# Kernel tuning notes

Measured on AMD Instinct MI355X. Metric: run time of the kernel, lower is better.

## Reference

```python
import jax, jax.numpy as jnp
import numpy as np

T, D = 2048, 2048
N = 16
DN, DR, DV = 128, 64, 128   # qk_nope_head_dim, qk_rope_head_dim, v_head_dim
RQ, RKV = 1536, 512         # q_lora_rank, kv_lora_rank
EPS = 1e-6
THETA = 10000.0


def rmsnorm(x, scale, eps=EPS):
    var = jnp.mean(jnp.square(x), axis=-1, keepdims=True)
    return x * jax.lax.rsqrt(var + eps) * scale


def apply_rope(x, pos, theta=THETA):
    # x: [T, dr] or [T, N, dr]; rotate-half (NeoX) rotary embedding
    dr = x.shape[-1]
    half = dr // 2
    inv_freq = theta ** (-jnp.arange(half, dtype=jnp.float32) / half)
    freqs = pos.astype(jnp.float32)[:, None] * inv_freq  # [T, half]
    cos, sin = jnp.cos(freqs), jnp.sin(freqs)
    while cos.ndim < x.ndim:
        cos, sin = cos[:, None, :], sin[:, None, :]
    x1, x2 = jnp.split(x, 2, axis=-1)
    return jnp.concatenate([x1 * cos - x2 * sin, x2 * cos + x1 * sin], axis=-1).astype(x.dtype)


def setup_inputs() -> dict:
    key = jax.random.key(0)
    ks = jax.random.split(key, 6)
    s = 0.02
    return {
        'x': jax.random.normal(ks[0], (T, D), jnp.float32),
        'positions': jnp.arange(T, dtype=jnp.int32),
        'w_q_a': jax.random.normal(ks[1], (D, RQ), jnp.float32) * s,
        'q_a_norm': jnp.ones((RQ,), jnp.float32),
        'w_q_b': jax.random.normal(ks[2], (RQ, N * (DN + DR)), jnp.float32) * s,
        'w_kv_a': jax.random.normal(ks[3], (D, RKV + DR), jnp.float32) * s,
        'kv_a_norm': jnp.ones((RKV,), jnp.float32),
        'w_kv_b': jax.random.normal(ks[4], (RKV, N * (DN + DV)), jnp.float32) * s,
        'w_o': jax.random.normal(ks[5], (N * DV, D), jnp.float32) * s,
    }


def reference(x, positions, w_q_a, q_a_norm, w_q_b, w_kv_a, kv_a_norm, w_kv_b, w_o):
    t = x.shape[0]
    # --- low-rank Q projection ---
    q_c = rmsnorm(x @ w_q_a, q_a_norm)                      # [T, RQ]
    q = (q_c @ w_q_b).reshape(t, N, DN + DR)                # [T, N, DN+DR]
    q_nope, q_pe = q[..., :DN], q[..., DN:]
    q_pe = apply_rope(q_pe, positions)                      # [T, N, DR]
    # --- low-rank KV projection with shared rope key (MQA-style k_pe) ---
    kv = x @ w_kv_a                                          # [T, RKV+DR]
    kv_c, k_pe = kv[:, :RKV], kv[:, RKV:]
    kv_c = rmsnorm(kv_c, kv_a_norm)                          # [T, RKV]
    k_pe = apply_rope(k_pe, positions)                       # [T, DR]
    kvb = (kv_c @ w_kv_b).reshape(t, N, DN + DV)             # [T, N, DN+DV]
    k_nope, v = kvb[..., :DN], kvb[..., DN:]
    # --- causal attention, scale over full qk head dim ---
    scale = (DN + DR) ** -0.5
    scores = (jnp.einsum('tnh,snh->nts', q_nope, k_nope)
              + jnp.einsum('tnh,sh->nts', q_pe, k_pe)) * scale   # [N, T, T]
    causal = positions[:, None] >= positions[None, :]
    scores = jnp.where(causal[None, :, :], scores, jnp.finfo(scores.dtype).min)
    p = jax.nn.softmax(scores, axis=-1)
    out = jnp.einsum('nts,snv->tnv', p, v).reshape(t, N * DV)
    return out @ w_o                                          # [T, D]
```

## Files before the change

### kernel.cpp

```cpp
#include <hip/hip_runtime.h>
#include <hip/hip_bf16.h>
#include <math.h>

#define T_TOK   2048
#define NHEADS  16
#define EPS_    1e-6f
#define THETA_  10000.0f

typedef __attribute__((ext_vector_type(8))) short short8v;
typedef __attribute__((ext_vector_type(4))) float f32x4;

__device__ inline unsigned short f2bf(float f) {
    union { float f; unsigned u; } v; v.f = f;
    unsigned r = v.u + 0x7fffu + ((v.u >> 16) & 1u);
    return (unsigned short)(r >> 16);
}

__device__ __forceinline__ void gload16(const unsigned short* src, unsigned short* lds) {
    __builtin_amdgcn_global_load_lds(
        (const __attribute__((address_space(1))) unsigned int*)src,
        (__attribute__((address_space(3))) unsigned int*)lds, 16, 0, 0);
}

__device__ inline float block_reduce(float v, bool is_max, float* sred) {
    #pragma unroll
    for (int off = 32; off > 0; off >>= 1) {
        float o = __shfl_down(v, off, 64);
        v = is_max ? fmaxf(v, o) : (v + o);
    }
    int tid = threadIdx.x;
    __syncthreads();
    if ((tid & 63) == 0) sred[tid >> 6] = v;
    __syncthreads();
    float r = sred[0];
    #pragma unroll
    for (int w = 1; w < 4; ++w) r = is_max ? fmaxf(r, sred[w]) : (r + sred[w]);
    return r;
}

__global__ __launch_bounds__(256) void conv_bf16(const float* __restrict__ in,
    unsigned short* __restrict__ out, int n4)
{
    int i = blockIdx.x * 256 + threadIdx.x;
    if (i >= n4) return;
    float4 v = ((const float4*)in)[i];
    ushort4 o;
    o.x = f2bf(v.x); o.y = f2bf(v.y); o.z = f2bf(v.z); o.w = f2bf(v.w);
    ((ushort4*)out)[i] = o;
}

__global__ __launch_bounds__(256) void wt_bf16(const float* __restrict__ W,
    unsigned short* __restrict__ Wt, int R, int C)
{
    __shared__ float tile[32][33];
    int c0 = blockIdx.x * 32, r0 = blockIdx.y * 32;
    int tx = threadIdx.x & 31, ty = threadIdx.x >> 5;
    #pragma unroll
    for (int i = 0; i < 4; ++i)
        tile[ty + i * 8][tx] = W[(size_t)(r0 + ty + i * 8) * C + c0 + tx];
    __syncthreads();
    #pragma unroll
    for (int i = 0; i < 4; ++i)
        Wt[(size_t)(c0 + ty + i * 8) * R + r0 + tx] = f2bf(tile[tx][ty + i * 8]);
}

template<bool BF16OUT>
__global__ __launch_bounds__(256) void gemm_bf16(
    const unsigned short* __restrict__ A,
    const unsigned short* __restrict__ Bt,
    void* __restrict__ Cv, int N, int K, int ldc)
{
    __shared__ __align__(16) unsigned short As[2][128 * 64];
    __shared__ __align__(16) unsigned short Bs[2][128 * 64];
    const int tid = threadIdx.x;
    const int lane = tid & 63, wid = tid >> 6;
    const int wr = wid >> 1, wc = wid & 1;
    const int lrow = lane & 15, lkg = lane >> 4;
    const int r0 = blockIdx.y * 128, c0 = blockIdx.x * 128;

    f32x4 acc[4][4];
    #pragma unroll
    for (int m = 0; m < 4; ++m)
        #pragma unroll
        for (int n = 0; n < 4; ++n) acc[m][n] = (f32x4)0.f;

    #define STAGE_GEMM(buf, k0)                                                   \
        {   _Pragma("unroll")                                                     \
            for (int p = 0; p < 4; ++p) {                                         \
                int u = p * 256 + tid;                                            \
                int r = u >> 3, cu = u & 7;                                       \
                int dst = (p * 256 + wid * 64) * 8;                               \
                gload16(A  + (size_t)(r0 + r) * K + (k0) + ((cu ^ (r & 7)) << 3), \
                        As[buf] + dst);                                           \
                gload16(Bt + (size_t)(c0 + r) * K + (k0) + ((cu ^ (r & 7)) << 3), \
                        Bs[buf] + dst);                                           \
            }                                                                     \
        }

    STAGE_GEMM(0, 0)

    const int nkt = K >> 6;
    int buf = 0;
    for (int kt = 0; kt < nkt; ++kt) {
        if (kt + 1 < nkt) {
            STAGE_GEMM(buf ^ 1, (kt + 1) << 6)
            asm volatile("s_waitcnt vmcnt(8)" ::: "memory");
        } else {
            asm volatile("s_waitcnt vmcnt(0)" ::: "memory");
        }
        __builtin_amdgcn_s_barrier();
        #pragma unroll
        for (int ks = 0; ks < 2; ++ks) {
            short8v af[4], bf[4];
            #pragma unroll
            for (int m = 0; m < 4; ++m) {
                int row = wr * 64 + m * 16 + lrow;
                af[m] = *(const short8v*)((char*)As[buf] + row * 128 + (((ks * 4 + lkg) ^ (row & 7)) << 4));
            }
            #pragma unroll
            for (int n = 0; n < 4; ++n) {
                int row = wc * 64 + n * 16 + lrow;
                bf[n] = *(const short8v*)((char*)Bs[buf] + row * 128 + (((ks * 4 + lkg) ^ (row & 7)) << 4));
            }
            #pragma unroll
            for (int m = 0; m < 4; ++m)
                #pragma unroll
                for (int n = 0; n < 4; ++n)
                    acc[m][n] = __builtin_amdgcn_mfma_f32_16x16x32_bf16(af[m], bf[n], acc[m][n], 0, 0, 0);
        }
        __builtin_amdgcn_s_barrier();
        buf ^= 1;
    }
    #undef STAGE_GEMM

    #pragma unroll
    for (int m = 0; m < 4; ++m) {
        int grow = r0 + wr * 64 + m * 16 + lkg * 4;
        #pragma unroll
        for (int n = 0; n < 4; ++n) {
            int gcol = c0 + wc * 64 + n * 16 + lrow;
            if (gcol < N) {
                #pragma unroll
                for (int j = 0; j < 4; ++j) {
                    if (BF16OUT)
                        ((unsigned short*)Cv)[(size_t)(grow + j) * ldc + gcol] = f2bf(acc[m][n][j]);
                    else
                        ((float*)Cv)[(size_t)(grow + j) * ldc + gcol] = acc[m][n][j];
                }
            }
        }
    }
}

__global__ __launch_bounds__(256) void rms_kv(const float* __restrict__ qkv,
    const float* __restrict__ gq, const float* __restrict__ gkv,
    const int* __restrict__ positions, unsigned short* __restrict__ q_cb,
    unsigned short* __restrict__ kv_cb, float* __restrict__ kpe)
{
    __shared__ float sred[4];
    int row = blockIdx.x, tid = threadIdx.x;
    const float* p = qkv + (size_t)row * 2112;

    float ss = 0.f;
    for (int i = tid; i < 1536; i += 256) { float v = p[i]; ss += v * v; }
    ss = block_reduce(ss, false, sred);
    float sc = rsqrtf(ss / 1536.0f + EPS_);
    for (int i = tid; i < 1536; i += 256)
        q_cb[(size_t)row * 1536 + i] = f2bf(p[i] * sc * gq[i]);

    float s2 = 0.f;
    for (int i = tid; i < 512; i += 256) { float v = p[1536 + i]; s2 += v * v; }
    s2 = block_reduce(s2, false, sred);
    float sc2 = rsqrtf(s2 / 512.0f + EPS_);
    for (int i = tid; i < 512; i += 256)
        kv_cb[(size_t)row * 512 + i] = f2bf(p[1536 + i] * sc2 * gkv[i]);

    if (tid < 32) {
        int i = tid;
        float pos = (float)positions[row];
        float inv = powf(THETA_, -(float)i / 32.0f);
        float ang = pos * inv;
        float c = cosf(ang), s = sinf(ang);
        float x1 = p[2048 + i], x2 = p[2080 + i];
        kpe[(size_t)row * 64 + i]      = x1 * c - x2 * s;
        kpe[(size_t)row * 64 + 32 + i] = x2 * c + x1 * s;
    }
}

__global__ __launch_bounds__(192) void rope_qb(const float* __restrict__ q,
    const int* __restrict__ positions, unsigned short* __restrict__ qb)
{
    int t = blockIdx.x, d = threadIdx.x;
    const float scale = 0.07216878364870323f;
    float c = 1.f, s = 0.f;
    if (d >= 128) {
        int i = (d - 128) & 31;
        float pos = (float)positions[t];
        float inv = powf(THETA_, -(float)i / 32.0f);
        float ang = pos * inv;
        c = cosf(ang); s = sinf(ang);
    }
    #pragma unroll 4
    for (int n = 0; n < 16; ++n) {
        const float* p = q + (size_t)t * 3072 + n * 192;
        float v;
        if (d < 128)      v = p[d];
        else if (d < 160) v = p[d] * c - p[d + 32] * s;
        else              v = p[d] * c + p[d - 32] * s;
        qb[((size_t)t * 16 + n) * 192 + d] = f2bf(v * scale);
    }
}

__global__ __launch_bounds__(256) void repack_k(const unsigned short* __restrict__ kvbb,
    const float* __restrict__ kpe, unsigned short* __restrict__ Kc)
{
    int t = blockIdx.x, tid = threadIdx.x;
    int n = tid >> 4;
    int c8 = tid & 15;
    short8v v = *(const short8v*)(kvbb + ((size_t)t * 16 + n) * 256 + c8 * 8);
    *(short8v*)(Kc + ((size_t)n * 2048 + t) * 192 + c8 * 8) = v;
    int i4 = (tid & 15) * 4;
    float4 p = *(const float4*)(kpe + (size_t)t * 64 + i4);
    ushort4 o; o.x = f2bf(p.x); o.y = f2bf(p.y); o.z = f2bf(p.z); o.w = f2bf(p.w);
    *(ushort4*)(Kc + ((size_t)n * 2048 + t) * 192 + 128 + i4) = o;
}

__global__ __launch_bounds__(256) void repack_vt(const unsigned short* __restrict__ kvbb,
    unsigned short* __restrict__ Vtc)
{
    __shared__ unsigned short tile[64][72];
    int t0 = blockIdx.x * 64;
    int n = blockIdx.y >> 1, dv0 = (blockIdx.y & 1) * 64;
    int tid = threadIdx.x;
    for (int u = tid; u < 512; u += 256) {
        int t = u >> 3, c8 = u & 7;
        short8v v = *(const short8v*)(kvbb + ((size_t)(t0 + t) * 16 + n) * 256 + 128 + dv0 + c8 * 8);
        *(short8v*)(&tile[t][c8 * 8]) = v;
    }
    __syncthreads();
    for (int u = tid; u < 512; u += 256) {
        int dv = u & 63, t8 = u >> 6;
        short8v v;
        #pragma unroll
        for (int e = 0; e < 8; ++e) v[e] = (short)tile[t8 * 8 + e][dv];
        *(short8v*)(Vtc + ((size_t)n * 128 + dv0 + dv) * 2048 + t0 + t8 * 8) = v;
    }
}

#define QBLK  64
#define KVBLK 64
#define NCH   3

__global__ __launch_bounds__(256) void attn_part(
    const unsigned short* __restrict__ qb,
    const unsigned short* __restrict__ Kc,
    const unsigned short* __restrict__ Vtc,
    unsigned short* __restrict__ Opart,
    float2* __restrict__ Ml)
{
    __shared__ __align__(16) unsigned short Ks[2][KVBLK * 192];
    __shared__ __align__(16) unsigned short Vt[128 * KVBLK];
    __shared__ __align__(16) unsigned short Ps[4][16 * KVBLK];

    const int bid = blockIdx.x;
    const int xcd = bid & 7;
    const int j   = bid >> 3;
    const int n   = xcd * 2 + (j >= 96);
    const int jj  = (j >= 96) ? j - 96 : j;
    const int qt  = 31 - (jj / NCH);
    const int ch  = jj % NCH;

    const int nt  = qt + 1;
    const int csz = (nt + NCH - 1) / NCH;
    const int tstart = ch * csz;
    if (tstart >= nt) return;
    const int tend = min(tstart + csz, nt);

    const int tid = threadIdx.x;
    const int lane = tid & 63, wid = tid >> 6;
    const int lrow = lane & 15;
    const int lkg  = lane >> 4;
    const int q0 = qt * QBLK;
    const int qrow_g = q0 + wid * 16 + lrow;
    const int pidx = ((n * 32 + qt) * NCH + ch);

    const unsigned short* Kh = Kc  + (size_t)n * 2048 * 192;
    const unsigned short* Vh = Vtc + (size_t)n * 128 * 2048;

    int koff[6], voff[4];
    #pragma unroll
    for (int p = 0; p < 6; ++p) {
        int u = p * 256 + tid;
        int row = u / 24, c8 = u % 24;
        koff[p] = row * 192 + ((c8 ^ (row & 7)) << 3);
    }
    #pragma unroll
    for (int p = 0; p < 4; ++p) {
        int u = p * 256 + tid;
        int dv = u >> 3, c8 = u & 7;
        voff[p] = dv * 2048 + ((c8 ^ (dv & 7)) << 3);
    }

    short8v qf[6];
    {
        const unsigned short* qrow = qb + ((size_t)qrow_g * 16 + n) * 192;
        #pragma unroll
        for (int ds = 0; ds < 6; ++ds)
            qf[ds] = *(const short8v*)(qrow + ds * 32 + lkg * 8);
    }

    f32x4 oacc[8];
    #pragma unroll
    for (int i = 0; i < 8; ++i) oacc[i] = (f32x4)0.f;
    float mrow = -3e38f;
    float lsum = 0.f;

    #pragma unroll
    for (int p = 0; p < 6; ++p)
        gload16(Kh + (size_t)tstart * KVBLK * 192 + koff[p], Ks[0] + (p * 256 + wid * 64) * 8);
    #pragma unroll
    for (int p = 0; p < 4; ++p)
        gload16(Vh + tstart * KVBLK + voff[p], Vt + (p * 256 + wid * 64) * 8);

    int buf = 0;
    for (int tile = tstart; tile < tend; ++tile) {
        const int s0 = tile * KVBLK;
        const bool more = (tile + 1 < tend);

        if (more) {
            #pragma unroll
            for (int p = 0; p < 6; ++p)
                gload16(Kh + (size_t)(s0 + KVBLK) * 192 + koff[p],
                        Ks[buf ^ 1] + (p * 256 + wid * 64) * 8);
            asm volatile("s_waitcnt vmcnt(10)" ::: "memory");
        } else {
            asm volatile("s_waitcnt vmcnt(4)" ::: "memory");
        }
        __builtin_amdgcn_s_barrier();

        f32x4 sacc[4];
        #pragma unroll
        for (int ct = 0; ct < 4; ++ct) sacc[ct] = (f32x4)0.f;
        __builtin_amdgcn_s_setprio(1);
        #pragma unroll
        for (int ds = 0; ds < 6; ++ds) {
            #pragma unroll
            for (int ct = 0; ct < 4; ++ct) {
                int krow = ct * 16 + lrow;
                int byte = (krow * 384 + ds * 64 + lkg * 16) ^ ((krow & 7) << 4);
                short8v kf = *(const short8v*)((char*)Ks[buf] + byte);
                sacc[ct] = __builtin_amdgcn_mfma_f32_16x16x32_bf16(kf, qf[ds], sacc[ct], 0, 0, 0);
            }
        }
        __builtin_amdgcn_s_setprio(0);

        #pragma unroll
        for (int ct = 0; ct < 4; ++ct) {
            #pragma unroll
            for (int jq = 0; jq < 4; ++jq) {
                int key = s0 + ct * 16 + lkg * 4 + jq;
                if (key > qrow_g) sacc[ct][jq] = -3e38f;
            }
        }

        float tm = -3e38f;
        #pragma unroll
        for (int ct = 0; ct < 4; ++ct) {
            float a = fmaxf(sacc[ct][0], sacc[ct][1]);
            float b = fmaxf(sacc[ct][2], sacc[ct][3]);
            tm = fmaxf(tm, fmaxf(a, b));
        }
        tm = fmaxf(tm, __shfl_xor(tm, 16, 64));
        tm = fmaxf(tm, __shfl_xor(tm, 32, 64));

        const bool grow = !__all(tm <= mrow);
        float corr = 1.f;
        if (grow) {
            float mn = fmaxf(mrow, tm);
            corr = __expf(mrow - mn);
            mrow = mn;
        }

        float psum = 0.f;
        unsigned short pb[4][4];
        #pragma unroll
        for (int ct = 0; ct < 4; ++ct)
            #pragma unroll
            for (int jq = 0; jq < 4; ++jq) {
                float sv = sacc[ct][jq];
                float p = (sv > -1e37f) ? __expf(sv - mrow) : 0.f;
                psum += p;
                pb[ct][jq] = f2bf(p);
            }
        psum += __shfl_xor(psum, 16, 64);
        psum += __shfl_xor(psum, 32, 64);
        lsum = grow ? (lsum * corr + psum) : (lsum + psum);

        if (grow) {
            float corr4[4];
            #pragma unroll
            for (int jq = 0; jq < 4; ++jq)
                corr4[jq] = __shfl(corr, (lane & 48) | (lkg * 4 + jq), 64);
            #pragma unroll
            for (int dt = 0; dt < 8; ++dt)
                #pragma unroll
                for (int jq = 0; jq < 4; ++jq) oacc[dt][jq] *= corr4[jq];
        }

        #pragma unroll
        for (int ct = 0; ct < 4; ++ct) {
            int c0k = ct * 16 + lkg * 4;
            int byte = ((lrow * 64 + c0k) * 2) ^ ((lrow & 7) << 4);
            uint2 w;
            w.x = (unsigned)pb[ct][0] | ((unsigned)pb[ct][1] << 16);
            w.y = (unsigned)pb[ct][2] | ((unsigned)pb[ct][3] << 16);
            *(uint2*)((char*)Ps[wid] + byte) = w;
        }

        if (more) asm volatile("s_waitcnt vmcnt(6)" ::: "memory");
        else      asm volatile("s_waitcnt vmcnt(0)" ::: "memory");
        __builtin_amdgcn_s_barrier();

        __builtin_amdgcn_s_setprio(1);
        #pragma unroll
        for (int ks = 0; ks < 2; ++ks) {
            int abyte = ((lrow * 64 + ks * 32 + lkg * 8) * 2) ^ ((lrow & 7) << 4);
            short8v af = *(const short8v*)((char*)Ps[wid] + abyte);
            #pragma unroll
            for (int dt = 0; dt < 8; ++dt) {
                int vrow = dt * 16 + lrow;
                int byte = ((vrow * 128 + ks * 64 + lkg * 16)) ^ ((vrow & 7) << 4);
                short8v bf = *(const short8v*)((char*)Vt + byte);
                oacc[dt] = __builtin_amdgcn_mfma_f32_16x16x32_bf16(af, bf, oacc[dt], 0, 0, 0);
            }
        }
        __builtin_amdgcn_s_setprio(0);

        __builtin_amdgcn_s_barrier();
        if (more) {
            #pragma unroll
            for (int p = 0; p < 4; ++p)
                gload16(Vh + (s0 + KVBLK) + voff[p], Vt + (p * 256 + wid * 64) * 8);
        }
        buf ^= 1;
    }

    #pragma unroll
    for (int dt = 0; dt < 8; ++dt)
        #pragma unroll
        for (int jq = 0; jq < 4; ++jq) {
            int row = wid * 16 + lkg * 4 + jq;
            Opart[(size_t)pidx * 8192 + row * 128 + dt * 16 + lrow] = f2bf(oacc[dt][jq]);
        }
    if (lkg == 0)
        Ml[(size_t)pidx * 64 + wid * 16 + lrow] = make_float2(mrow, lsum);
}

__global__ __launch_bounds__(256) void attn_combine(
    const unsigned short* __restrict__ Opart, const float2* __restrict__ Ml,
    unsigned short* __restrict__ aob)
{
    const int bid = blockIdx.x;
    const int head = bid >> 5, qt = bid & 31;
    const int nt = qt + 1, csz = (nt + NCH - 1) / NCH;
    const int nch = (nt + csz - 1) / csz;
    const int tid = threadIdx.x;
    const int r = tid >> 2, qc = tid & 3;
    const int base = (head * 32 + qt) * NCH;

    float mi[NCH], li[NCH];
    float m = -3e38f;
    #pragma unroll
    for (int i = 0; i < NCH; ++i) {
        mi[i] = -3e38f; li[i] = 0.f;
        if (i < nch) {
            float2 v = Ml[(size_t)(base + i) * 64 + r];
            mi[i] = v.x; li[i] = v.y;
            m = fmaxf(m, v.x);
        }
    }
    float acc[32];
    #pragma unroll
    for (int u = 0; u < 32; ++u) acc[u] = 0.f;
    float l = 0.f;
    #pragma unroll
    for (int i = 0; i < NCH; ++i) {
        if (i < nch) {
            float w = __expf(mi[i] - m);
            l += w * li[i];
            const unsigned short* op = Opart + (size_t)(base + i) * 8192 + r * 128 + qc * 32;
            #pragma unroll
            for (int u = 0; u < 4; ++u) {
                short8v v8 = *(const short8v*)(op + u * 8);
                #pragma unroll
                for (int e = 0; e < 8; ++e)
                    acc[u * 8 + e] += w * __uint_as_float(((unsigned)(unsigned short)v8[e]) << 16);
            }
        }
    }
    float invl = 1.0f / l;
    unsigned short* dst = aob + (size_t)(qt * 64 + r) * 2048 + head * 128 + qc * 32;
    #pragma unroll
    for (int u = 0; u < 4; ++u) {
        short8v o8;
        #pragma unroll
        for (int e = 0; e < 8; ++e) o8[e] = (short)f2bf(acc[u * 8 + e] * invl);
        *(short8v*)(dst + u * 8) = o8;
    }
}

extern "C" void kernel_launch(void* const* d_in, const int* in_sizes, int n_in,
                              void* d_out, int out_size, void* d_ws, size_t ws_size,
                              hipStream_t stream)
{
    const float* x         = (const float*)d_in[0];
    const int*   positions = (const int*)  d_in[1];
    const float* w_q_a     = (const float*)d_in[2];
    const float* q_a_norm  = (const float*)d_in[3];
    const float* w_q_b     = (const float*)d_in[4];
    const float* w_kv_a    = (const float*)d_in[5];
    const float* kv_a_norm = (const float*)d_in[6];
    const float* w_kv_b    = (const float*)d_in[7];
    const float* w_o       = (const float*)d_in[8];
    float* out = (float*)d_out;

    char* base = (char*)d_ws;
    float* q = (float*)base;
    unsigned short* Kc  = (unsigned short*)base;
    unsigned short* Vtc = Kc + (size_t)16 * 2048 * 192;
    char* pR1 = base + (size_t)2048 * 3072 * 4;
    float* qkv_c = (float*)pR1;
    unsigned short* kvbb  = (unsigned short*)pR1;
    unsigned short* Opart = (unsigned short*)pR1;
    float2* Ml = (float2*)(pR1 + (size_t)1536 * 8192 * 2);
    char* pR2 = pR1 + (size_t)1536 * 8192 * 2 + (size_t)1536 * 64 * 8;
    unsigned short* q_cb  = (unsigned short*)pR2;
    unsigned short* kv_cb = q_cb + (size_t)2048 * 1536;
    float* kpe = (float*)(kv_cb + (size_t)2048 * 512);
    char* pR3 = pR2 + (size_t)2048 * 1536 * 2 + (size_t)2048 * 512 * 2 + (size_t)2048 * 64 * 4;
    unsigned short* xb  = (unsigned short*)pR3;
    unsigned short* aob = xb;
    char* pR4 = pR3 + (size_t)2048 * 2048 * 2;
    unsigned short* qb = (unsigned short*)pR4;
    char* pR5 = pR4 + (size_t)2048 * 3072 * 2;
    unsigned short* wbuf = (unsigned short*)pR5;

    dim3 blk(256);

    conv_bf16<<<(2048 * 2048 / 4 + 255) / 256, blk, 0, stream>>>(x, xb, 2048 * 2048 / 4);

    wt_bf16<<<dim3(1536 / 32, 2048 / 32), blk, 0, stream>>>(w_q_a, wbuf, 2048, 1536);
    wt_bf16<<<dim3(576 / 32, 2048 / 32), blk, 0, stream>>>(w_kv_a, wbuf + (size_t)1536 * 2048, 2048, 576);
    gemm_bf16<false><<<dim3(17, 16), blk, 0, stream>>>(xb, wbuf, qkv_c, 2112, 2048, 2112);
    rms_kv<<<2048, blk, 0, stream>>>(qkv_c, q_a_norm, kv_a_norm, positions, q_cb, kv_cb, kpe);

    wt_bf16<<<dim3(3072 / 32, 1536 / 32), blk, 0, stream>>>(w_q_b, wbuf, 1536, 3072);
    gemm_bf16<false><<<dim3(3072 / 128, 16), blk, 0, stream>>>(q_cb, wbuf, q, 3072, 1536, 3072);
    rope_qb<<<2048, dim3(192), 0, stream>>>(q, positions, qb);

    wt_bf16<<<dim3(4096 / 32, 512 / 32), blk, 0, stream>>>(w_kv_b, wbuf, 512, 4096);
    gemm_bf16<true><<<dim3(4096 / 128, 16), blk, 0, stream>>>(kv_cb, wbuf, kvbb, 4096, 512, 4096);

    repack_k<<<2048, blk, 0, stream>>>(kvbb, kpe, Kc);
    repack_vt<<<dim3(32, 32), blk, 0, stream>>>(kvbb, Vtc);

    attn_part<<<1536, blk, 0, stream>>>(qb, Kc, Vtc, Opart, Ml);
    attn_combine<<<512, blk, 0, stream>>>(Opart, Ml, aob);

    wt_bf16<<<dim3(2048 / 32, 2048 / 32), blk, 0, stream>>>(w_o, wbuf, 2048, 2048);
    gemm_bf16<false><<<dim3(2048 / 128, 16), blk, 0, stream>>>(aob, wbuf, out, 2048, 2048, 2048);
}
```

Before: 241.0 us.

## Fuse K/V repacking into kv_b GEMM epilogue and single-buffer K in attention

Adds a gemm_kv kernel whose epilogue writes K_nope directly into the per-head Kc layout and V transposed into Vtc. This removes the bf16 kvbb intermediate and the separate repack_k/repack_vt kernels. The rope part of K is written by a new small kpe_kc kernel. Attention also drops K double buffering: both K and V for the next tile are now issued after the PV stage. That frees LDS, possibly for more occupancy, but exposes K load latency at the start of each tile.

Result: faster. 230.7 us (-4.3%).

```diff
diff --git a/kernel.cpp b/kernel.cpp
--- a/kernel.cpp
+++ b/kernel.cpp
@@ -63,6 +63,57 @@
     for (int i = 0; i < 4; ++i)
         Wt[(size_t)(c0 + ty + i * 8) * R + r0 + tx] = f2bf(tile[tx][ty + i * 8]);
 }
+
+#define STAGE_GEMM(buf, k0)                                                   \
+    {   _Pragma("unroll")                                                     \
+        for (int p = 0; p < 4; ++p) {                                         \
+            int u = p * 256 + tid;                                            \
+            int r = u >> 3, cu = u & 7;                                       \
+            int dst = (p * 256 + wid * 64) * 8;                               \
+            gload16(A  + (size_t)(r0 + r) * K + (k0) + ((cu ^ (r & 7)) << 3), \
+                    As[buf] + dst);                                           \
+            gload16(Bt + (size_t)(c0 + r) * K + (k0) + ((cu ^ (r & 7)) << 3), \
+                    Bs[buf] + dst);                                           \
+        }                                                                     \
+    }
+
+#define GEMM_BODY()                                                           \
+    STAGE_GEMM(0, 0)                                                          \
+    const int nkt = K >> 6;                                                   \
+    int buf = 0;                                                              \
+    for (int kt = 0; kt < nkt; ++kt) {                                        \
+        if (kt + 1 < nkt) {                                                   \
+            STAGE_GEMM(buf ^ 1, (kt + 1) << 6)                                \
+            asm volatile("s_waitcnt vmcnt(8)" ::: "memory");                  \
+        } else {                                                              \
+            asm volatile("s_waitcnt vmcnt(0)" ::: "memory");                  \
+        }                                                                     \
+        __builtin_amdgcn_s_barrier();                                         \
+        _Pragma("unroll")                                                     \
+        for (int ks = 0; ks < 2; ++ks) {                                      \
+            short8v af[4], bf[4];                                             \
+            _Pragma("unroll")                                                 \
+            for (int m = 0; m < 4; ++m) {                                     \
+                int row = wr * 64 + m * 16 + lrow;                            \
+                af[m] = *(const short8v*)((char*)As[buf] + row * 128 +        \
+                        (((ks * 4 + lkg) ^ (row & 7)) << 4));                 \
+            }                                                                 \
+            _Pragma("unroll")                                                 \
+            for (int n = 0; n < 4; ++n) {                                     \
+                int row = wc * 64 + n * 16 + lrow;                            \
+                bf[n] = *(const short8v*)((char*)Bs[buf] + row * 128 +        \
+                        (((ks * 4 + lkg) ^ (row & 7)) << 4));                 \
+            }                                                                 \
+            _Pragma("unroll")                                                 \
+            for (int m = 0; m < 4; ++m)                                       \
+                _Pragma("unroll")                                             \
+                for (int n = 0; n < 4; ++n)                                   \
+                    acc[m][n] = __builtin_amdgcn_mfma_f32_16x16x32_bf16(      \
+                        af[m], bf[n], acc[m][n], 0, 0, 0);                    \
+        }                                                                     \
+        __builtin_amdgcn_s_barrier();                                         \
+        buf ^= 1;                                                             \
+    }
 
 template<bool BF16OUT>
 __global__ __launch_bounds__(256) void gemm_bf16(
@@ -84,54 +135,7 @@
         #pragma unroll
         for (int n = 0; n < 4; ++n) acc[m][n] = (f32x4)0.f;
 
-    #define STAGE_GEMM(buf, k0)                                                   \
-        {   _Pragma("unroll")                                                     \
-            for (int p = 0; p < 4; ++p) {                                         \
-                int u = p * 256 + tid;                                            \
-                int r = u >> 3, cu = u & 7;                                       \
-                int dst = (p * 256 + wid * 64) * 8;                               \
-                gload16(A  + (size_t)(r0 + r) * K + (k0) + ((cu ^ (r & 7)) << 3), \
-                        As[buf] + dst);                                           \
-                gload16(Bt + (size_t)(c0 + r) * K + (k0) + ((cu ^ (r & 7)) << 3), \
-                        Bs[buf] + dst);                                           \
-            }                                                                     \
-        }
-
-    STAGE_GEMM(0, 0)
-
-    const int nkt = K >> 6;
-    int buf = 0;
-    for (int kt = 0; kt < nkt; ++kt) {
-        if (kt + 1 < nkt) {
-            STAGE_GEMM(buf ^ 1, (kt + 1) << 6)
-            asm volatile("s_waitcnt vmcnt(8)" ::: "memory");
-        } else {
-            asm volatile("s_waitcnt vmcnt(0)" ::: "memory");
-        }
-        __builtin_amdgcn_s_barrier();
-        #pragma unroll
-        for (int ks = 0; ks < 2; ++ks) {
-            short8v af[4], bf[4];
-            #pragma unroll
-            for (int m = 0; m < 4; ++m) {
-                int row = wr * 64 + m * 16 + lrow;
-                af[m] = *(const short8v*)((char*)As[buf] + row * 128 + (((ks * 4 + lkg) ^ (row & 7)) << 4));
-            }
-            #pragma unroll
-            for (int n = 0; n < 4; ++n) {
-                int row = wc * 64 + n * 16 + lrow;
-                bf[n] = *(const short8v*)((char*)Bs[buf] + row * 128 + (((ks * 4 + lkg) ^ (row & 7)) << 4));
-            }
-            #pragma unroll
-            for (int m = 0; m < 4; ++m)
-                #pragma unroll
-                for (int n = 0; n < 4; ++n)
-                    acc[m][n] = __builtin_amdgcn_mfma_f32_16x16x32_bf16(af[m], bf[n], acc[m][n], 0, 0, 0);
-        }
-        __builtin_amdgcn_s_barrier();
-        buf ^= 1;
-    }
-    #undef STAGE_GEMM
+    GEMM_BODY()
 
     #pragma unroll
     for (int m = 0; m < 4; ++m) {
@@ -152,6 +156,50 @@
     }
 }
 
+__global__ __launch_bounds__(256) void gemm_kv(
+    const unsigned short* __restrict__ A,
+    const unsigned short* __restrict__ Bt,
+    unsigned short* __restrict__ Kc,
+    unsigned short* __restrict__ Vtc)
+{
+    __shared__ __align__(16) unsigned short As[2][128 * 64];
+    __shared__ __align__(16) unsigned short Bs[2][128 * 64];
+    const int tid = threadIdx.x;
+    const int lane = tid & 63, wid = tid >> 6;
+    const int wr = wid >> 1, wc = wid & 1;
+    const int lrow = lane & 15, lkg = lane >> 4;
+    const int r0 = blockIdx.y * 128, c0 = blockIdx.x * 128;
+    const int K = 512;
+
+    f32x4 acc[4][4];
+    #pragma unroll
+    for (int m = 0; m < 4; ++m)
+        #pragma unroll
+        for (int n = 0; n < 4; ++n) acc[m][n] = (f32x4)0.f;
+
+    GEMM_BODY()
+
+    #pragma unroll
+    for (int m = 0; m < 4; ++m) {
+        int grow = r0 + wr * 64 + m * 16 + lkg * 4;
+        #pragma unroll
+        for (int n = 0; n < 4; ++n) {
+            int gcol = c0 + wc * 64 + n * 16 + lrow;
+            int head = gcol >> 8, c = gcol & 255;
+            if (c < 128) {
+                #pragma unroll
+                for (int j = 0; j < 4; ++j)
+                    Kc[((size_t)head * 2048 + grow + j) * 192 + c] = f2bf(acc[m][n][j]);
+            } else {
+                ushort4 o;
+                o.x = f2bf(acc[m][n][0]); o.y = f2bf(acc[m][n][1]);
+                o.z = f2bf(acc[m][n][2]); o.w = f2bf(acc[m][n][3]);
+                *(ushort4*)(Vtc + ((size_t)head * 128 + (c - 128)) * 2048 + grow) = o;
+            }
+        }
+    }
+}
+
 __global__ __launch_bounds__(256) void rms_kv(const float* __restrict__ qkv,
     const float* __restrict__ gq, const float* __restrict__ gkv,
     const int* __restrict__ positions, unsigned short* __restrict__ q_cb,
@@ -187,6 +235,16 @@
     }
 }
 
+__global__ __launch_bounds__(256) void kpe_kc(const float* __restrict__ kpe,
+    unsigned short* __restrict__ Kc)
+{
+    int t = blockIdx.x, tid = threadIdx.x;
+    int n = tid >> 4, i4 = (tid & 15) * 4;
+    float4 p = *(const float4*)(kpe + (size_t)t * 64 + i4);
+    ushort4 o; o.x = f2bf(p.x); o.y = f2bf(p.y); o.z = f2bf(p.z); o.w = f2bf(p.w);
+    *(ushort4*)(Kc + ((size_t)n * 2048 + t) * 192 + 128 + i4) = o;
+}
+
 __global__ __launch_bounds__(192) void rope_qb(const float* __restrict__ q,
     const int* __restrict__ positions, unsigned short* __restrict__ qb)
 {
@@ -211,42 +269,6 @@
     }
 }
 
-__global__ __launch_bounds__(256) void repack_k(const unsigned short* __restrict__ kvbb,
-    const float* __restrict__ kpe, unsigned short* __restrict__ Kc)
-{
-    int t = blockIdx.x, tid = threadIdx.x;
-    int n = tid >> 4;
-    int c8 = tid & 15;
-    short8v v = *(const short8v*)(kvbb + ((size_t)t * 16 + n) * 256 + c8 * 8);
-    *(short8v*)(Kc + ((size_t)n * 2048 + t) * 192 + c8 * 8) = v;
-    int i4 = (tid & 15) * 4;
-    float4 p = *(const float4*)(kpe + (size_t)t * 64 + i4);
-    ushort4 o; o.x = f2bf(p.x); o.y = f2bf(p.y); o.z = f2bf(p.z); o.w = f2bf(p.w);
-    *(ushort4*)(Kc + ((size_t)n * 2048 + t) * 192 + 128 + i4) = o;
-}
-
-__global__ __launch_bounds__(256) void repack_vt(const unsigned short* __restrict__ kvbb,
-    unsigned short* __restrict__ Vtc)
-{
-    __shared__ unsigned short tile[64][72];
-    int t0 = blockIdx.x * 64;
-    int n = blockIdx.y >> 1, dv0 = (blockIdx.y & 1) * 64;
-    int tid = threadIdx.x;
-    for (int u = tid; u < 512; u += 256) {
-        int t = u >> 3, c8 = u & 7;
-        short8v v = *(const short8v*)(kvbb + ((size_t)(t0 + t) * 16 + n) * 256 + 128 + dv0 + c8 * 8);
-        *(short8v*)(&tile[t][c8 * 8]) = v;
-    }
-    __syncthreads();
-    for (int u = tid; u < 512; u += 256) {
-        int dv = u & 63, t8 = u >> 6;
-        short8v v;
-        #pragma unroll
-        for (int e = 0; e < 8; ++e) v[e] = (short)tile[t8 * 8 + e][dv];
-        *(short8v*)(Vtc + ((size_t)n * 128 + dv0 + dv) * 2048 + t0 + t8 * 8) = v;
-    }
-}
-
 #define QBLK  64
 #define KVBLK 64
 #define NCH   3
@@ -258,7 +280,7 @@
     unsigned short* __restrict__ Opart,
     float2* __restrict__ Ml)
 {
-    __shared__ __align__(16) unsigned short Ks[2][KVBLK * 192];
+    __shared__ __align__(16) unsigned short Ks[KVBLK * 192];
     __shared__ __align__(16) unsigned short Vt[128 * KVBLK];
     __shared__ __align__(16) unsigned short Ps[4][16 * KVBLK];
 
@@ -317,25 +339,16 @@
 
     #pragma unroll
     for (int p = 0; p < 6; ++p)
-        gload16(Kh + (size_t)tstart * KVBLK * 192 + koff[p], Ks[0] + (p * 256 + wid * 64) * 8);
+        gload16(Kh + (size_t)tstart * KVBLK * 192 + koff[p], Ks + (p * 256 + wid * 64) * 8);
     #pragma unroll
     for (int p = 0; p < 4; ++p)
         gload16(Vh + tstart * KVBLK + voff[p], Vt + (p * 256 + wid * 64) * 8);
 
-    int buf = 0;
     for (int tile = tstart; tile < tend; ++tile) {
         const int s0 = tile * KVBLK;
         const bool more = (tile + 1 < tend);
 
-        if (more) {
-            #pragma unroll
-            for (int p = 0; p < 6; ++p)
-                gload16(Kh + (size_t)(s0 + KVBLK) * 192 + koff[p],
-                        Ks[buf ^ 1] + (p * 256 + wid * 64) * 8);
-            asm volatile("s_waitcnt vmcnt(10)" ::: "memory");
-        } else {
-            asm volatile("s_waitcnt vmcnt(4)" ::: "memory");
-        }
+        asm volatile("s_waitcnt vmcnt(4)" ::: "memory");
         __builtin_amdgcn_s_barrier();
 
         f32x4 sacc[4];
@@ -348,7 +361,7 @@
             for (int ct = 0; ct < 4; ++ct) {
                 int krow = ct * 16 + lrow;
                 int byte = (krow * 384 + ds * 64 + lkg * 16) ^ ((krow & 7) << 4);
-                short8v kf = *(const short8v*)((char*)Ks[buf] + byte);
+                short8v kf = *(const short8v*)((char*)Ks + byte);
                 sacc[ct] = __builtin_amdgcn_mfma_f32_16x16x32_bf16(kf, qf[ds], sacc[ct], 0, 0, 0);
             }
         }
@@ -417,8 +430,7 @@
             *(uint2*)((char*)Ps[wid] + byte) = w;
         }
 
-        if (more) asm volatile("s_waitcnt vmcnt(6)" ::: "memory");
-        else      asm volatile("s_waitcnt vmcnt(0)" ::: "memory");
+        asm volatile("s_waitcnt vmcnt(0)" ::: "memory");
         __builtin_amdgcn_s_barrier();
 
         __builtin_amdgcn_s_setprio(1);
@@ -438,11 +450,14 @@
 
         __builtin_amdgcn_s_barrier();
         if (more) {
+            const int s1 = s0 + KVBLK;
+            #pragma unroll
+            for (int p = 0; p < 6; ++p)
+                gload16(Kh + (size_t)s1 * 192 + koff[p], Ks + (p * 256 + wid * 64) * 8);
             #pragma unroll
             for (int p = 0; p < 4; ++p)
-                gload16(Vh + (s0 + KVBLK) + voff[p], Vt + (p * 256 + wid * 64) * 8);
-        }
-        buf ^= 1;
+                gload16(Vh + s1 + voff[p], Vt + (p * 256 + wid * 64) * 8);
+        }
     }
 
     #pragma unroll
@@ -530,7 +545,6 @@
     unsigned short* Vtc = Kc + (size_t)16 * 2048 * 192;
     char* pR1 = base + (size_t)2048 * 3072 * 4;
     float* qkv_c = (float*)pR1;
-    unsigned short* kvbb  = (unsigned short*)pR1;
     unsigned short* Opart = (unsigned short*)pR1;
     float2* Ml = (float2*)(pR1 + (size_t)1536 * 8192 * 2);
     char* pR2 = pR1 + (size_t)1536 * 8192 * 2 + (size_t)1536 * 64 * 8;
@@ -558,11 +572,10 @@
     gemm_bf16<false><<<dim3(3072 / 128, 16), blk, 0, stream>>>(q_cb, wbuf, q, 3072, 1536, 3072);
     rope_qb<<<2048, dim3(192), 0, stream>>>(q, positions, qb);
 
+    kpe_kc<<<2048, blk, 0, stream>>>(kpe, Kc);
+
     wt_bf16<<<dim3(4096 / 32, 512 / 32), blk, 0, stream>>>(w_kv_b, wbuf, 512, 4096);
-    gemm_bf16<true><<<dim3(4096 / 128, 16), blk, 0, stream>>>(kv_cb, wbuf, kvbb, 4096, 512, 4096);
-
-    repack_k<<<2048, blk, 0, stream>>>(kvbb, kpe, Kc);
-    repack_vt<<<dim3(32, 32), blk, 0, stream>>>(kvbb, Vtc);
+    gemm_kv<<<dim3(4096 / 128, 16), blk, 0, stream>>>(kv_cb, wbuf, Kc, Vtc);
 
     attn_part<<<1536, blk, 0, stream>>>(qb, Kc, Vtc, Opart, Ml);
     attn_combine<<<512, blk, 0, stream>>>(Opart, Ml, aob);
```
